# Performance work log

Hardware: AMD Instinct MI355X
Metric: run time of the kernel (lower is better)

## Reference

```python
import jax, jax.numpy as jnp
import numpy as np

N_NODES = 100_000
N_EDGES = 1_600_000
N_FEAT = 64
HIDDEN = 64
BIOPRINT = 2048
N_GRAPHS = 1024


def setup_inputs() -> dict:
    key = jax.random.key(0)
    ks = jax.random.split(key, 12)
    x = jax.random.normal(ks[0], (N_NODES, N_FEAT), jnp.float32)
    edge_index = jax.random.randint(ks[1], (2, N_EDGES), 0, N_NODES, dtype=jnp.int64)
    batch = jnp.sort(jax.random.randint(ks[2], (N_NODES,), 0, N_GRAPHS, dtype=jnp.int64))
    def lin(k, fan_in, fan_out):
        s = 1.0 / np.sqrt(fan_in)
        return jax.random.uniform(k, (fan_in, fan_out), jnp.float32, -s, s)
    W1 = lin(ks[3], N_FEAT, HIDDEN)
    b1 = jnp.zeros((HIDDEN,), jnp.float32)
    W2 = lin(ks[4], HIDDEN, HIDDEN)
    b2 = jnp.zeros((HIDDEN,), jnp.float32)
    W3 = lin(ks[5], HIDDEN, HIDDEN)
    b3 = jnp.zeros((HIDDEN,), jnp.float32)
    Wd = lin(ks[6], HIDDEN, BIOPRINT)
    bd = jax.random.uniform(ks[7], (BIOPRINT,), jnp.float32, -1.0 / np.sqrt(HIDDEN), 1.0 / np.sqrt(HIDDEN))
    return {"x": x, "edge_index": edge_index, "batch": batch,
            "W1": W1, "b1": b1, "W2": W2, "b2": b2, "W3": W3, "b3": b3,
            "Wd": Wd, "bd": bd}


def reference(x, edge_index, batch, W1, b1, W2, b2, W3, b3, Wd, bd):
    n = x.shape[0]
    src, dst = edge_index[0], edge_index[1]
    # GCN symmetric normalization with self-loops: deg = in-degree + 1
    ones_e = jnp.ones(src.shape[0], x.dtype)
    deg = jax.ops.segment_sum(ones_e, dst, num_segments=n) + 1.0
    dinv = jax.lax.rsqrt(deg)  # deg >= 1 always
    self_norm = (dinv * dinv)[:, None]
    edge_norm = (dinv[src] * dinv[dst])[:, None]

    def gcn_conv(h, W, b):
        hw = h @ W  # [N, out]
        agg = jax.ops.segment_sum(hw[src] * edge_norm, dst, num_segments=n)
        return agg + hw * self_norm + b  # self-loop handled analytically

    h = jax.nn.relu(gcn_conv(x, W1, b1))
    h = jax.nn.relu(gcn_conv(h, W2, b2))
    h = gcn_conv(h, W3, b3)

    # global_mean_pool over graph ids
    cnt = jax.ops.segment_sum(jnp.ones(n, x.dtype), batch, num_segments=N_GRAPHS)
    pooled = jax.ops.segment_sum(h, batch, num_segments=N_GRAPHS) / jnp.maximum(cnt, 1.0)[:, None]

    # dropout(p=0.5) is identity in eval mode
    logits = pooled @ Wd + bd
    probs = jax.nn.softmax(logits, axis=-1)
    return (probs >= 0.5).astype(x.dtype)
```

## Files before the change

kernel.cpp:

```cpp
#include <hip/hip_runtime.h>
#include <hip/hip_fp16.h>
#include <math.h>

#define N_NODES   100000
#define N_EDGES   1600000
#define N_FEAT    64
#define HIDDEN    64
#define BIOPRINT  2048
#define N_GRAPHS  1024

#define SENTINEL  N_NODES
#define ELL_STRIDE 64

#define N_E4 (N_EDGES / 4)
#define DEG_BLOCKS ((N_E4 + 255) / 256)
#define FILL_BLOCKS DEG_BLOCKS
#define MM1_BLOCKS (N_NODES / 32)
#define GS_BLOCKS  5

__device__ __forceinline__ __half2 shx_h2(__half2 v, int m) {
    int x = __shfl_xor(*(int*)&v, m);
    return *(__half2*)&x;
}

__device__ __forceinline__ void stage_w_perm(const float* __restrict__ W, float* sW, int t) {
    const float4* W4 = (const float4*)W;
    for (int i = t; i < 1024; i += 256) {
        float4 w = W4[i];
        int k = i >> 4;
        int c4 = (i & 15) * 4;
        int base = (k >> 2) * 256 + (k & 3);
        sW[base + (c4 + 0) * 4] = w.x;
        sW[base + (c4 + 1) * 4] = w.y;
        sW[base + (c4 + 2) * 4] = w.z;
        sW[base + (c4 + 3) * 4] = w.w;
    }
}

__global__ __launch_bounds__(256) void k_degmm(
        const int* __restrict__ dst, int* __restrict__ deg, int* __restrict__ rank,
        const float* __restrict__ x, const float* __restrict__ W,
        __half* __restrict__ hw) {
    int bid = blockIdx.x;
    int t = threadIdx.x;
    if (bid < DEG_BLOCKS) {
        int tid = bid * 256 + t;
        if (tid < N_E4) {
            int4 d4 = ((const int4*)dst)[tid];
            int4 r4;
            r4.x = atomicAdd(&deg[d4.x], 1);
            r4.y = atomicAdd(&deg[d4.y], 1);
            r4.z = atomicAdd(&deg[d4.z], 1);
            r4.w = atomicAdd(&deg[d4.w], 1);
            ((int4*)rank)[tid] = r4;
        }
        return;
    }
    __shared__ float sW[64 * 64];
    __shared__ float sA[32 * 64];
    stage_w_perm(W, sW, t);
    int row0 = (bid - DEG_BLOCKS) * 32;
    ((float4*)sA)[t]       = ((const float4*)x)[row0 * 16 + t];
    ((float4*)sA)[t + 256] = ((const float4*)x)[row0 * 16 + t + 256];
    __syncthreads();
    int wave = t >> 6, lane = t & 63;
    const float4* sWp = (const float4*)sW;
    float sum[8] = {0.f, 0.f, 0.f, 0.f, 0.f, 0.f, 0.f, 0.f};
#pragma unroll
    for (int k4 = 0; k4 < 16; ++k4) {
        float4 w4 = sWp[k4 * 64 + lane];
#pragma unroll
        for (int hh = 0; hh < 8; ++hh) {
            float4 a4 = ((const float4*)&sA[(wave * 8 + hh) * 64])[k4];
            sum[hh] = fmaf(a4.x, w4.x, sum[hh]);
            sum[hh] = fmaf(a4.y, w4.y, sum[hh]);
            sum[hh] = fmaf(a4.z, w4.z, sum[hh]);
            sum[hh] = fmaf(a4.w, w4.w, sum[hh]);
        }
    }
#pragma unroll
    for (int hh = 0; hh < 8; ++hh) {
        int row = row0 + wave * 8 + hh;
        hw[(size_t)row * 64 + lane] = __float2half_rn(sum[hh]);
    }
}

__global__ __launch_bounds__(256) void k_fillprep(
        const int* __restrict__ src, const int* __restrict__ dst,
        const int* __restrict__ rank, int* __restrict__ colELL,
        const int* __restrict__ deg, float* __restrict__ dinv,
        __half* __restrict__ hw,
        const int* __restrict__ batch, int* __restrict__ gstart) {
    int bid = blockIdx.x, t = threadIdx.x;
    if (bid < FILL_BLOCKS) {
        int tid = bid * 256 + t;
        if (tid < N_E4) {
            int4 d4 = ((const int4*)dst)[tid];
            int4 r4 = ((const int4*)rank)[tid];
            int4 s4 = ((const int4*)src)[tid];
            colELL[d4.x * ELL_STRIDE + (r4.x & 63)] = s4.x;
            colELL[d4.y * ELL_STRIDE + (r4.y & 63)] = s4.y;
            colELL[d4.z * ELL_STRIDE + (r4.z & 63)] = s4.z;
            colELL[d4.w * ELL_STRIDE + (r4.w & 63)] = s4.w;
        }
        return;
    }
    bid -= FILL_BLOCKS;
    if (bid < MM1_BLOCKS) {
        int row0 = bid * 32;
        int row = row0 + (t >> 3);
        float di = rsqrtf((float)deg[row] + 1.0f);
        uint4* p = (uint4*)hw;
        uint4 v = p[(size_t)row * 8 + (t & 7)];
        __half2* h2 = (__half2*)&v;
#pragma unroll
        for (int c = 0; c < 4; ++c) {
            float2 f = __half22float2(h2[c]);
            h2[c] = __halves2half2(__float2half_rn(f.x * di), __float2half_rn(f.y * di));
        }
        p[(size_t)row * 8 + (t & 7)] = v;
        if ((t & 7) == 0) dinv[row] = di;
        if (t < 32) {
            int r2 = row0 + t;
            int dv = deg[r2]; if (dv > 64) dv = 64;
            int vp = (dv + 7) & ~7;
            for (int j = dv; j < vp; ++j) colELL[r2 * ELL_STRIDE + j] = SENTINEL;
        }
        return;
    }
    int g = (bid - MM1_BLOCKS) * 256 + t;
    if (g > N_GRAPHS) return;
    if (g == N_GRAPHS) { gstart[g] = N_NODES; return; }
    int lo = 0, hi = N_NODES;
    while (lo < hi) { int mid = (lo + hi) >> 1; if (batch[mid] < g) lo = mid + 1; else hi = mid; }
    gstart[g] = lo;
}

__device__ __forceinline__ void gather2x4(
        const int* __restrict__ col, const uint4* __restrict__ hv,
        int rs, int re, int slot, int sub, float f[8]) {
    __half2 a0 = __float2half2_rn(0.f), a1 = a0, a2 = a0, a3 = a0;
    __half2 c0 = a0, c1 = a0, c2 = a0, c3 = a0;
    for (int e = rs; e < re; e += 8) {
        int s0 = __builtin_nontemporal_load(&col[e + slot]);
        int s1 = __builtin_nontemporal_load(&col[e + 2 + slot]);
        int s2 = __builtin_nontemporal_load(&col[e + 4 + slot]);
        int s3 = __builtin_nontemporal_load(&col[e + 6 + slot]);
        uint4 u0 = hv[(size_t)s0 * 8 + sub];
        uint4 u1 = hv[(size_t)s1 * 8 + sub];
        uint4 u2 = hv[(size_t)s2 * 8 + sub];
        uint4 u3 = hv[(size_t)s3 * 8 + sub];
        a0 = __hadd2(a0, *(__half2*)&u0.x); a1 = __hadd2(a1, *(__half2*)&u0.y);
        a2 = __hadd2(a2, *(__half2*)&u0.z); a3 = __hadd2(a3, *(__half2*)&u0.w);
        c0 = __hadd2(c0, *(__half2*)&u1.x); c1 = __hadd2(c1, *(__half2*)&u1.y);
        c2 = __hadd2(c2, *(__half2*)&u1.z); c3 = __hadd2(c3, *(__half2*)&u1.w);
        a0 = __hadd2(a0, *(__half2*)&u2.x); a1 = __hadd2(a1, *(__half2*)&u2.y);
        a2 = __hadd2(a2, *(__half2*)&u2.z); a3 = __hadd2(a3, *(__half2*)&u2.w);
        c0 = __hadd2(c0, *(__half2*)&u3.x); c1 = __hadd2(c1, *(__half2*)&u3.y);
        c2 = __hadd2(c2, *(__half2*)&u3.z); c3 = __hadd2(c3, *(__half2*)&u3.w);
    }
    a0 = __hadd2(a0, c0); a1 = __hadd2(a1, c1);
    a2 = __hadd2(a2, c2); a3 = __hadd2(a3, c3);
    a0 = __hadd2(a0, shx_h2(a0, 8));
    a1 = __hadd2(a1, shx_h2(a1, 8));
    a2 = __hadd2(a2, shx_h2(a2, 8));
    a3 = __hadd2(a3, shx_h2(a3, 8));
    float2 f0 = __half22float2(a0), f1 = __half22float2(a1);
    float2 f2 = __half22float2(a2), f3 = __half22float2(a3);
    f[0] = f0.x; f[1] = f0.y; f[2] = f1.x; f[3] = f1.y;
    f[4] = f2.x; f[5] = f2.y; f[6] = f3.x; f[7] = f3.y;
}

__global__ __launch_bounds__(256) void k_gmm(
        const int* __restrict__ deg, const int* __restrict__ col,
        const float* __restrict__ dinv, const float* __restrict__ b,
        const __half* __restrict__ hw_in, const float* __restrict__ W,
        __half* __restrict__ hw_out) {
    __shared__ float sW[64 * 64];
    __shared__ float sA[16 * 64];
    int t = threadIdx.x;
    stage_w_perm(W, sW, t);
    __syncthreads();

    int wave = t >> 6, lane = t & 63;
    int quarter = lane >> 4, slot = (lane >> 3) & 1, sub = lane & 7;
    int i0 = blockIdx.x * 16 + wave * 4;
    int i = i0 + quarter;
    float di = dinv[i];
    int dv = deg[i]; if (dv > 64) dv = 64;
    int rs = i * ELL_STRIDE;
    int re = rs + ((dv + 7) & ~7);
    const uint4* hv = (const uint4*)hw_in;

    float f[8];
    gather2x4(col, hv, rs, re, slot, sub, f);

    uint4 us = hv[(size_t)i * 8 + sub];
    float2 s0 = __half22float2(*(__half2*)&us.x);
    float2 s1 = __half22float2(*(__half2*)&us.y);
    float2 s2 = __half22float2(*(__half2*)&us.z);
    float2 s3 = __half22float2(*(__half2*)&us.w);
    float sf[8] = {s0.x, s0.y, s1.x, s1.y, s2.x, s2.y, s3.x, s3.y};
    float4 ba = ((const float4*)b)[sub * 2];
    float4 bb = ((const float4*)b)[sub * 2 + 1];
    float bf[8] = {ba.x, ba.y, ba.z, ba.w, bb.x, bb.y, bb.z, bb.w};
    if (slot == 0) {
        float r[8];
#pragma unroll
        for (int k = 0; k < 8; ++k) r[k] = fmaxf(fmaf(di, f[k] + sf[k], bf[k]), 0.f);
        *(float4*)&sA[(wave * 4 + quarter) * 64 + sub * 8]     = make_float4(r[0], r[1], r[2], r[3]);
        *(float4*)&sA[(wave * 4 + quarter) * 64 + sub * 8 + 4] = make_float4(r[4], r[5], r[6], r[7]);
    }

    const float4* sWp = (const float4*)sW;
    float sum[4] = {0.f, 0.f, 0.f, 0.f};
#pragma unroll
    for (int k4 = 0; k4 < 16; ++k4) {
        float4 w4 = sWp[k4 * 64 + lane];
#pragma unroll
        for (int hh = 0; hh < 4; ++hh) {
            float4 a4 = ((const float4*)&sA[(wave * 4 + hh) * 64])[k4];
            sum[hh] = fmaf(a4.x, w4.x, sum[hh]);
            sum[hh] = fmaf(a4.y, w4.y, sum[hh]);
            sum[hh] = fmaf(a4.z, w4.z, sum[hh]);
            sum[hh] = fmaf(a4.w, w4.w, sum[hh]);
        }
    }
#pragma unroll
    for (int hh = 0; hh < 4; ++hh)
        hw_out[(size_t)(i0 + hh) * 64 + lane] = __float2half_rn(sum[hh] * dinv[i0 + hh]);
}

__global__ __launch_bounds__(256) void k_gather3(
        const int* __restrict__ deg, const int* __restrict__ col,
        const float* __restrict__ dinv, const float* __restrict__ b,
        const __half* __restrict__ hw_in, __half* __restrict__ conv) {
    int t = threadIdx.x;
    int wave = t >> 6, lane = t & 63;
    int quarter = lane >> 4, slot = (lane >> 3) & 1, sub = lane & 7;
    int i = blockIdx.x * 16 + wave * 4 + quarter;
    float di = dinv[i];
    int dv = deg[i]; if (dv > 64) dv = 64;
    int rs = i * ELL_STRIDE;
    int re = rs + ((dv + 7) & ~7);
    const uint4* hv = (const uint4*)hw_in;

    float f[8];
    gather2x4(col, hv, rs, re, slot, sub, f);

    if (slot == 0) {
        uint4 us = hv[(size_t)i * 8 + sub];
        float2 s0 = __half22float2(*(__half2*)&us.x);
        float2 s1 = __half22float2(*(__half2*)&us.y);
        float2 s2 = __half22float2(*(__half2*)&us.z);
        float2 s3 = __half22float2(*(__half2*)&us.w);
        float sf[8] = {s0.x, s0.y, s1.x, s1.y, s2.x, s2.y, s3.x, s3.y};
        float4 ba = ((const float4*)b)[sub * 2];
        float4 bb = ((const float4*)b)[sub * 2 + 1];
        float bf[8] = {ba.x, ba.y, ba.z, ba.w, bb.x, bb.y, bb.z, bb.w};
        uint4 o;
        __half2* oh = (__half2*)&o;
#pragma unroll
        for (int c = 0; c < 4; ++c) {
            float r0 = fmaf(di, f[2 * c] + sf[2 * c], bf[2 * c]);
            float r1 = fmaf(di, f[2 * c + 1] + sf[2 * c + 1], bf[2 * c + 1]);
            oh[c] = __halves2half2(__float2half_rn(r0), __float2half_rn(r1));
        }
        ((uint4*)conv)[(size_t)i * 8 + sub] = o;
    }
}

__global__ __launch_bounds__(256) void k_dense(
        const __half* __restrict__ conv, const int* __restrict__ gstart,
        const float* __restrict__ Wd, const float* __restrict__ bd,
        float* __restrict__ out) {
    __shared__ float sred[4][64];
    __shared__ float sp[64];
    __shared__ float rmax[4];
    __shared__ float rsum[4];
    int t = threadIdx.x;
    int wave = t >> 6, lane = t & 63;
    int g = blockIdx.x;
    int n0 = gstart[g], n1 = gstart[g + 1];

    int fp = lane & 31;
    int par = lane >> 5;
    const __half2* conv2 = (const __half2*)conv;
    float2 acc2 = make_float2(0.f, 0.f);
    for (int i = n0 + wave * 2 + par; i < n1; i += 8) {
        float2 f = __half22float2(conv2[(size_t)i * 32 + fp]);
        acc2.x += f.x; acc2.y += f.y;
    }
    acc2.x += __shfl_xor(acc2.x, 32);
    acc2.y += __shfl_xor(acc2.y, 32);
    if (lane < 32) { sred[wave][2 * fp] = acc2.x; sred[wave][2 * fp + 1] = acc2.y; }
    __syncthreads();
    if (t < 64) {
        int n = n1 - n0;
        float s = sred[0][t] + sred[1][t] + sred[2][t] + sred[3][t];
        sp[t] = (n > 0) ? s / (float)n : 0.f;
    }
    __syncthreads();

    float acc[8];
#pragma unroll
    for (int r = 0; r < 8; ++r) acc[r] = bd[r * 256 + t];
    for (int k = 0; k < 64; ++k) {
        float h = sp[k];
#pragma unroll
        for (int r = 0; r < 8; ++r)
            acc[r] = fmaf(h, Wd[k * BIOPRINT + r * 256 + t], acc[r]);
    }

    float m = acc[0];
#pragma unroll
    for (int r = 1; r < 8; ++r) m = fmaxf(m, acc[r]);
#pragma unroll
    for (int off = 32; off > 0; off >>= 1) m = fmaxf(m, __shfl_xor(m, off));
    if (lane == 0) rmax[wave] = m;
    __syncthreads();
    m = fmaxf(fmaxf(rmax[0], rmax[1]), fmaxf(rmax[2], rmax[3]));

    float s = 0.f;
#pragma unroll
    for (int r = 0; r < 8; ++r) { acc[r] = expf(acc[r] - m); s += acc[r]; }
#pragma unroll
    for (int off = 32; off > 0; off >>= 1) s += __shfl_xor(s, off);
    if (lane == 0) rsum[wave] = s;
    __syncthreads();
    s = rsum[0] + rsum[1] + rsum[2] + rsum[3];

#pragma unroll
    for (int r = 0; r < 8; ++r) {
        float p = acc[r] / s;
        out[(size_t)g * BIOPRINT + r * 256 + t] = (p >= 0.5f) ? 1.0f : 0.0f;
    }
}


extern "C" void kernel_launch(void* const* d_in, const int* in_sizes, int n_in,
                              void* d_out, int out_size, void* d_ws, size_t ws_size,
                              hipStream_t stream) {
    const float* x     = (const float*)d_in[0];
    const int*   ei    = (const int*)d_in[1];
    const int*   batch = (const int*)d_in[2];
    const float* W1 = (const float*)d_in[3];
    const float* b1 = (const float*)d_in[4];
    const float* W2 = (const float*)d_in[5];
    const float* b2 = (const float*)d_in[6];
    const float* W3 = (const float*)d_in[7];
    const float* b3 = (const float*)d_in[8];
    const float* Wd = (const float*)d_in[9];
    const float* bd = (const float*)d_in[10];
    float* out = (float*)d_out;

    const int* src = ei;
    const int* dst = ei + N_EDGES;

    char* ws = (char*)d_ws;
    size_t off = 0;
    auto alloc = [&](size_t bytes) {
        void* p = ws + off;
        off += (bytes + 255) & ~(size_t)255;
        return p;
    };
    int*    deg    = (int*)alloc(N_NODES * sizeof(int));
    float*  dinv   = (float*)alloc(N_NODES * sizeof(float));
    int*    rank   = (int*)alloc((size_t)N_EDGES * sizeof(int));
    int*    gstart = (int*)alloc((N_GRAPHS + 1) * sizeof(int));
    int*    colELL = (int*)alloc((size_t)N_NODES * ELL_STRIDE * sizeof(int));
    __half* bufA   = (__half*)alloc((size_t)(N_NODES + 1) * HIDDEN * sizeof(__half));
    __half* bufB   = (__half*)alloc((size_t)(N_NODES + 1) * HIDDEN * sizeof(__half));
    __half* conv   = (__half*)alloc((size_t)N_NODES * HIDDEN * sizeof(__half));

    hipMemsetAsync(deg, 0, N_NODES * sizeof(int), stream);
    hipMemsetAsync(bufA + (size_t)N_NODES * HIDDEN, 0, HIDDEN * sizeof(__half), stream);
    hipMemsetAsync(bufB + (size_t)N_NODES * HIDDEN, 0, HIDDEN * sizeof(__half), stream);

    k_degmm<<<DEG_BLOCKS + MM1_BLOCKS, 256, 0, stream>>>(dst, deg, rank, x, W1, bufA);
    k_fillprep<<<FILL_BLOCKS + MM1_BLOCKS + GS_BLOCKS, 256, 0, stream>>>(
        src, dst, rank, colELL, deg, dinv, bufA, batch, gstart);

    const int g16_grid = N_NODES / 16;
    k_gmm<<<g16_grid, 256, 0, stream>>>(deg, colELL, dinv, b1, bufA, W2, bufB);
    k_gmm<<<g16_grid, 256, 0, stream>>>(deg, colELL, dinv, b2, bufB, W3, bufA);
    k_gather3<<<g16_grid, 256, 0, stream>>>(deg, colELL, dinv, b3, bufA, conv);
    k_dense<<<N_GRAPHS, 256, 0, stream>>>(conv, gstart, Wd, bd, out);
}
```

Baseline: 349.2 us.

## Move first matmul into fill kernel with fused dinv scaling; unroll gather by 16

The first-layer x@W1 matmul moves out of the degree-count kernel into the ELL fill kernel. Since degrees are final by then, dinv can be applied directly at store time, which removes the separate read-modify-write pass over hw. The edge gather now processes 16 ELL slots per iteration instead of 8, with padding rounded to 16, to keep more loads in flight. The cost is more sentinel padding work for low-degree nodes, higher register pressure in the gather, and a degree kernel that no longer overlaps with the matmul.

Result: faster. 338.4 us (-3.1%).

```diff
diff --git a/kernel.cpp b/kernel.cpp
--- a/kernel.cpp
+++ b/kernel.cpp
@@ -37,58 +37,25 @@
     }
 }
 
-__global__ __launch_bounds__(256) void k_degmm(
-        const int* __restrict__ dst, int* __restrict__ deg, int* __restrict__ rank,
-        const float* __restrict__ x, const float* __restrict__ W,
-        __half* __restrict__ hw) {
-    int bid = blockIdx.x;
-    int t = threadIdx.x;
-    if (bid < DEG_BLOCKS) {
-        int tid = bid * 256 + t;
-        if (tid < N_E4) {
-            int4 d4 = ((const int4*)dst)[tid];
-            int4 r4;
-            r4.x = atomicAdd(&deg[d4.x], 1);
-            r4.y = atomicAdd(&deg[d4.y], 1);
-            r4.z = atomicAdd(&deg[d4.z], 1);
-            r4.w = atomicAdd(&deg[d4.w], 1);
-            ((int4*)rank)[tid] = r4;
-        }
-        return;
-    }
-    __shared__ float sW[64 * 64];
-    __shared__ float sA[32 * 64];
-    stage_w_perm(W, sW, t);
-    int row0 = (bid - DEG_BLOCKS) * 32;
-    ((float4*)sA)[t]       = ((const float4*)x)[row0 * 16 + t];
-    ((float4*)sA)[t + 256] = ((const float4*)x)[row0 * 16 + t + 256];
-    __syncthreads();
-    int wave = t >> 6, lane = t & 63;
-    const float4* sWp = (const float4*)sW;
-    float sum[8] = {0.f, 0.f, 0.f, 0.f, 0.f, 0.f, 0.f, 0.f};
-#pragma unroll
-    for (int k4 = 0; k4 < 16; ++k4) {
-        float4 w4 = sWp[k4 * 64 + lane];
-#pragma unroll
-        for (int hh = 0; hh < 8; ++hh) {
-            float4 a4 = ((const float4*)&sA[(wave * 8 + hh) * 64])[k4];
-            sum[hh] = fmaf(a4.x, w4.x, sum[hh]);
-            sum[hh] = fmaf(a4.y, w4.y, sum[hh]);
-            sum[hh] = fmaf(a4.z, w4.z, sum[hh]);
-            sum[hh] = fmaf(a4.w, w4.w, sum[hh]);
-        }
-    }
-#pragma unroll
-    for (int hh = 0; hh < 8; ++hh) {
-        int row = row0 + wave * 8 + hh;
-        hw[(size_t)row * 64 + lane] = __float2half_rn(sum[hh]);
-    }
-}
-
-__global__ __launch_bounds__(256) void k_fillprep(
+__global__ __launch_bounds__(256) void k_deg(const int* __restrict__ dst,
+                                             int* __restrict__ deg,
+                                             int* __restrict__ rank) {
+    int tid = blockIdx.x * blockDim.x + threadIdx.x;
+    if (tid >= N_E4) return;
+    int4 d4 = ((const int4*)dst)[tid];
+    int4 r4;
+    r4.x = atomicAdd(&deg[d4.x], 1);
+    r4.y = atomicAdd(&deg[d4.y], 1);
+    r4.z = atomicAdd(&deg[d4.z], 1);
+    r4.w = atomicAdd(&deg[d4.w], 1);
+    ((int4*)rank)[tid] = r4;
+}
+
+__global__ __launch_bounds__(256) void k_fillmm(
         const int* __restrict__ src, const int* __restrict__ dst,
         const int* __restrict__ rank, int* __restrict__ colELL,
         const int* __restrict__ deg, float* __restrict__ dinv,
+        const float* __restrict__ x, const float* __restrict__ W,
         __half* __restrict__ hw,
         const int* __restrict__ batch, int* __restrict__ gstart) {
     int bid = blockIdx.x, t = threadIdx.x;
@@ -107,23 +74,40 @@
     }
     bid -= FILL_BLOCKS;
     if (bid < MM1_BLOCKS) {
+        __shared__ float sW[64 * 64];
+        __shared__ float sA[32 * 64];
+        stage_w_perm(W, sW, t);
         int row0 = bid * 32;
-        int row = row0 + (t >> 3);
-        float di = rsqrtf((float)deg[row] + 1.0f);
-        uint4* p = (uint4*)hw;
-        uint4 v = p[(size_t)row * 8 + (t & 7)];
-        __half2* h2 = (__half2*)&v;
-#pragma unroll
-        for (int c = 0; c < 4; ++c) {
-            float2 f = __half22float2(h2[c]);
-            h2[c] = __halves2half2(__float2half_rn(f.x * di), __float2half_rn(f.y * di));
-        }
-        p[(size_t)row * 8 + (t & 7)] = v;
-        if ((t & 7) == 0) dinv[row] = di;
+        ((float4*)sA)[t]       = ((const float4*)x)[row0 * 16 + t];
+        ((float4*)sA)[t + 256] = ((const float4*)x)[row0 * 16 + t + 256];
+        __syncthreads();
+        int wave = t >> 6, lane = t & 63;
+        const float4* sWp = (const float4*)sW;
+        float sum[8] = {0.f, 0.f, 0.f, 0.f, 0.f, 0.f, 0.f, 0.f};
+#pragma unroll
+        for (int k4 = 0; k4 < 16; ++k4) {
+            float4 w4 = sWp[k4 * 64 + lane];
+#pragma unroll
+            for (int hh = 0; hh < 8; ++hh) {
+                float4 a4 = ((const float4*)&sA[(wave * 8 + hh) * 64])[k4];
+                sum[hh] = fmaf(a4.x, w4.x, sum[hh]);
+                sum[hh] = fmaf(a4.y, w4.y, sum[hh]);
+                sum[hh] = fmaf(a4.z, w4.z, sum[hh]);
+                sum[hh] = fmaf(a4.w, w4.w, sum[hh]);
+            }
+        }
+#pragma unroll
+        for (int hh = 0; hh < 8; ++hh) {
+            int row = row0 + wave * 8 + hh;
+            float di = rsqrtf((float)deg[row] + 1.0f);
+            hw[(size_t)row * 64 + lane] = __float2half_rn(sum[hh] * di);
+        }
         if (t < 32) {
             int r2 = row0 + t;
-            int dv = deg[r2]; if (dv > 64) dv = 64;
-            int vp = (dv + 7) & ~7;
+            int dv = deg[r2];
+            dinv[r2] = rsqrtf((float)dv + 1.0f);
+            if (dv > 64) dv = 64;
+            int vp = (dv + 15) & ~15;
             for (int j = dv; j < vp; ++j) colELL[r2 * ELL_STRIDE + j] = SENTINEL;
         }
         return;
@@ -136,20 +120,28 @@
     gstart[g] = lo;
 }
 
-__device__ __forceinline__ void gather2x4(
+__device__ __forceinline__ void gather2x8(
         const int* __restrict__ col, const uint4* __restrict__ hv,
         int rs, int re, int slot, int sub, float f[8]) {
     __half2 a0 = __float2half2_rn(0.f), a1 = a0, a2 = a0, a3 = a0;
     __half2 c0 = a0, c1 = a0, c2 = a0, c3 = a0;
-    for (int e = rs; e < re; e += 8) {
+    for (int e = rs; e < re; e += 16) {
         int s0 = __builtin_nontemporal_load(&col[e + slot]);
         int s1 = __builtin_nontemporal_load(&col[e + 2 + slot]);
         int s2 = __builtin_nontemporal_load(&col[e + 4 + slot]);
         int s3 = __builtin_nontemporal_load(&col[e + 6 + slot]);
+        int s4 = __builtin_nontemporal_load(&col[e + 8 + slot]);
+        int s5 = __builtin_nontemporal_load(&col[e + 10 + slot]);
+        int s6 = __builtin_nontemporal_load(&col[e + 12 + slot]);
+        int s7 = __builtin_nontemporal_load(&col[e + 14 + slot]);
         uint4 u0 = hv[(size_t)s0 * 8 + sub];
         uint4 u1 = hv[(size_t)s1 * 8 + sub];
         uint4 u2 = hv[(size_t)s2 * 8 + sub];
         uint4 u3 = hv[(size_t)s3 * 8 + sub];
+        uint4 u4 = hv[(size_t)s4 * 8 + sub];
+        uint4 u5 = hv[(size_t)s5 * 8 + sub];
+        uint4 u6 = hv[(size_t)s6 * 8 + sub];
+        uint4 u7 = hv[(size_t)s7 * 8 + sub];
         a0 = __hadd2(a0, *(__half2*)&u0.x); a1 = __hadd2(a1, *(__half2*)&u0.y);
         a2 = __hadd2(a2, *(__half2*)&u0.z); a3 = __hadd2(a3, *(__half2*)&u0.w);
         c0 = __hadd2(c0, *(__half2*)&u1.x); c1 = __hadd2(c1, *(__half2*)&u1.y);
@@ -158,6 +150,14 @@
         a2 = __hadd2(a2, *(__half2*)&u2.z); a3 = __hadd2(a3, *(__half2*)&u2.w);
         c0 = __hadd2(c0, *(__half2*)&u3.x); c1 = __hadd2(c1, *(__half2*)&u3.y);
         c2 = __hadd2(c2, *(__half2*)&u3.z); c3 = __hadd2(c3, *(__half2*)&u3.w);
+        a0 = __hadd2(a0, *(__half2*)&u4.x); a1 = __hadd2(a1, *(__half2*)&u4.y);
+        a2 = __hadd2(a2, *(__half2*)&u4.z); a3 = __hadd2(a3, *(__half2*)&u4.w);
+        c0 = __hadd2(c0, *(__half2*)&u5.x); c1 = __hadd2(c1, *(__half2*)&u5.y);
+        c2 = __hadd2(c2, *(__half2*)&u5.z); c3 = __hadd2(c3, *(__half2*)&u5.w);
+        a0 = __hadd2(a0, *(__half2*)&u6.x); a1 = __hadd2(a1, *(__half2*)&u6.y);
+        a2 = __hadd2(a2, *(__half2*)&u6.z); a3 = __hadd2(a3, *(__half2*)&u6.w);
+        c0 = __hadd2(c0, *(__half2*)&u7.x); c1 = __hadd2(c1, *(__half2*)&u7.y);
+        c2 = __hadd2(c2, *(__half2*)&u7.z); c3 = __hadd2(c3, *(__half2*)&u7.w);
     }
     a0 = __hadd2(a0, c0); a1 = __hadd2(a1, c1);
     a2 = __hadd2(a2, c2); a3 = __hadd2(a3, c3);
@@ -189,11 +189,11 @@
     float di = dinv[i];
     int dv = deg[i]; if (dv > 64) dv = 64;
     int rs = i * ELL_STRIDE;
-    int re = rs + ((dv + 7) & ~7);
+    int re = rs + ((dv + 15) & ~15);
     const uint4* hv = (const uint4*)hw_in;
 
     float f[8];
-    gather2x4(col, hv, rs, re, slot, sub, f);
+    gather2x8(col, hv, rs, re, slot, sub, f);
 
     uint4 us = hv[(size_t)i * 8 + sub];
     float2 s0 = __half22float2(*(__half2*)&us.x);
@@ -242,11 +242,11 @@
     float di = dinv[i];
     int dv = deg[i]; if (dv > 64) dv = 64;
     int rs = i * ELL_STRIDE;
-    int re = rs + ((dv + 7) & ~7);
+    int re = rs + ((dv + 15) & ~15);
     const uint4* hv = (const uint4*)hw_in;
 
     float f[8];
-    gather2x4(col, hv, rs, re, slot, sub, f);
+    gather2x8(col, hv, rs, re, slot, sub, f);
 
     if (slot == 0) {
         uint4 us = hv[(size_t)i * 8 + sub];
@@ -377,9 +377,9 @@
     hipMemsetAsync(bufA + (size_t)N_NODES * HIDDEN, 0, HIDDEN * sizeof(__half), stream);
     hipMemsetAsync(bufB + (size_t)N_NODES * HIDDEN, 0, HIDDEN * sizeof(__half), stream);
 
-    k_degmm<<<DEG_BLOCKS + MM1_BLOCKS, 256, 0, stream>>>(dst, deg, rank, x, W1, bufA);
-    k_fillprep<<<FILL_BLOCKS + MM1_BLOCKS + GS_BLOCKS, 256, 0, stream>>>(
-        src, dst, rank, colELL, deg, dinv, bufA, batch, gstart);
+    k_deg<<<DEG_BLOCKS, 256, 0, stream>>>(dst, deg, rank);
+    k_fillmm<<<FILL_BLOCKS + MM1_BLOCKS + GS_BLOCKS, 256, 0, stream>>>(
+        src, dst, rank, colELL, deg, dinv, x, W1, bufA, batch, gstart);
 
     const int g16_grid = N_NODES / 16;
     k_gmm<<<g16_grid, 256, 0, stream>>>(deg, colELL, dinv, b1, bufA, W2, bufB);
```
